# Optimization experiments

Hardware: AMD Instinct MI355X
Metric: run time of the kernel (lower is better)

Reference implementation:

```python
import jax, jax.numpy as jnp
import numpy as np
from jax import lax

DN = ('NCHW', 'OIHW', 'NCHW')


def conv2d(x, w, b, pad):
    y = lax.conv_general_dilated(x, w, (1, 1), [(pad, pad), (pad, pad)], dimension_numbers=DN)
    return y + b[None, :, None, None]


def bilinear_sample(x, py, px):
    # x: [B,C,H,W]; py,px: [B,kk,H,W] fractional sample coords (zero outside).
    B, C, H, W = x.shape
    y0 = jnp.floor(py)
    x0 = jnp.floor(px)
    wy1 = py - y0
    wx1 = px - x0
    wy0 = 1.0 - wy1
    wx0 = 1.0 - wx1
    xf = x.reshape(B, C, H * W)

    def gather(yi, xi):
        valid = (yi >= 0) & (yi <= H - 1) & (xi >= 0) & (xi <= W - 1)
        yc = jnp.clip(yi, 0, H - 1).astype(jnp.int32)
        xc = jnp.clip(xi, 0, W - 1).astype(jnp.int32)
        idx = (yc * W + xc).reshape(B, -1)  # [B, kk*H*W]
        v = jax.vmap(lambda xb, ib: xb[:, ib])(xf, idx)  # [B,C,kk*H*W]
        v = v.reshape(B, C, *yi.shape[1:])
        return v * valid[:, None].astype(x.dtype)

    out = gather(y0, x0) * (wy0 * wx0)[:, None]
    out = out + gather(y0, x0 + 1.0) * (wy0 * wx1)[:, None]
    out = out + gather(y0 + 1.0, x0) * (wy1 * wx0)[:, None]
    out = out + gather(y0 + 1.0, x0 + 1.0) * (wy1 * wx1)[:, None]
    return out  # [B,C,kk,H,W]


def deform_branch(x, w_off, b_off, w_mask, b_mask, w_dcn, k):
    # offset/mask generator convs (kernel k, same padding), then DCNv2-style
    # modulated deformable conv (stride 1, dilation 1, groups 1, no bias).
    pad = k // 2
    kk = k * k
    B, C, H, W = x.shape
    offset = conv2d(x, w_off, b_off, pad)              # [B,2kk,H,W]
    mask = jax.nn.sigmoid(conv2d(x, w_mask, b_mask, pad))  # [B,kk,H,W]
    oy = offset[:, 0::2]  # y offsets per tap  [B,kk,H,W]
    ox = offset[:, 1::2]  # x offsets per tap
    iy, ix = jnp.meshgrid(jnp.arange(k), jnp.arange(k), indexing='ij')
    iy = iy.reshape(-1).astype(x.dtype)  # [kk]
    ix = ix.reshape(-1).astype(x.dtype)
    base_y = jnp.arange(H, dtype=x.dtype)[None, :, None] - pad + iy[:, None, None]  # [kk,H,1]
    base_x = jnp.arange(W, dtype=x.dtype)[None, None, :] - pad + ix[:, None, None]  # [kk,1,W]
    py = base_y[None] + oy  # [B,kk,H,W]
    px = base_x[None] + ox
    samp = bilinear_sample(x, py, px) * mask[:, None]  # [B,C,kk,H,W]
    wf = w_dcn.reshape(w_dcn.shape[0], w_dcn.shape[1], kk)  # [Cout,Cin,kk]
    return jnp.einsum('bckhw,ock->bohw', samp, wf)


def setup_inputs() -> dict:
    key = jax.random.key(0)
    B, Cin, Cout, H, W = 2, 64, 64, 80, 80
    ks = jax.random.split(key, 20)
    inp = {'x': jax.random.normal(ks[0], (B, Cin, H, W), dtype=jnp.float32)}
    i = 1
    for k in (3, 5, 7):
        kk = k * k
        inp[f'w_off{k}'] = jax.random.normal(ks[i], (2 * kk, Cin, k, k), dtype=jnp.float32) * 0.02
        inp[f'b_off{k}'] = jax.random.normal(ks[i + 1], (2 * kk,), dtype=jnp.float32) * 0.1
        inp[f'w_mask{k}'] = jax.random.normal(ks[i + 2], (kk, Cin, k, k), dtype=jnp.float32) * 0.02
        inp[f'b_mask{k}'] = jax.random.normal(ks[i + 3], (kk,), dtype=jnp.float32) * 0.1
        inp[f'w_dcn{k}'] = jax.random.normal(ks[i + 4], (Cout, Cin, k, k), dtype=jnp.float32) * (1.0 / np.sqrt(Cin * kk))
        i += 5
    return inp


def reference(x, w_off3, b_off3, w_mask3, b_mask3, w_dcn3,
              w_off5, b_off5, w_mask5, b_mask5, w_dcn5,
              w_off7, b_off7, w_mask7, b_mask7, w_dcn7):
    p1 = deform_branch(x, w_off3, b_off3, w_mask3, b_mask3, w_dcn3, 3)
    p2 = deform_branch(x, w_off5, b_off5, w_mask5, b_mask5, w_dcn5, 5)
    p3 = deform_branch(x, w_off7, b_off7, w_mask7, b_mask7, w_dcn7, 7)
    return jnp.concatenate([p1, p2, p3], axis=1)
```

## Files before the change

kernel.cpp:

```cpp
#include <hip/hip_runtime.h>
#include <math.h>

constexpr int B = 2, C = 64, H = 80, W = 80, HW = H * W, COUT = 64;
constexpr int NPIX = B * HW;

typedef __attribute__((ext_vector_type(8))) short short8;
typedef __attribute__((ext_vector_type(4))) float f32x4;
typedef __attribute__((ext_vector_type(2))) float f32x2;

__device__ inline ushort f2bf(float f) {
  unsigned u = __float_as_uint(f);
  unsigned r = u + 0x7fff + ((u >> 16) & 1);
  return (ushort)(r >> 16);
}

__device__ inline f32x2 unpack_bf2(unsigned u) {
  f32x2 r;
  r.x = __uint_as_float(u << 16);
  r.y = __uint_as_float(u & 0xffff0000u);
  return r;
}

__device__ inline unsigned bilin_pack(unsigned a, unsigned b, unsigned c,
                                      unsigned d, f32x2 c00, f32x2 c01,
                                      f32x2 c10, f32x2 c11) {
  f32x2 p = unpack_bf2(a) * c00;
  p += unpack_bf2(b) * c01;
  p += unpack_bf2(c) * c10;
  p += unpack_bf2(d) * c11;
  unsigned lo = __float_as_uint(p.x) + 0x8000u;
  unsigned hi = __float_as_uint(p.y) + 0x8000u;
  return __builtin_amdgcn_perm(hi, lo, 0x07060302);
}

__device__ __forceinline__ void gload_lds16(const ushort* g, ushort* s) {
  __builtin_amdgcn_global_load_lds(
      (const __attribute__((address_space(1))) void*)g,
      (__attribute__((address_space(3))) void*)s, 16, 0, 0);
}

template <int K, int NT>
__device__ void prep_body(int pb, int nblk, const float* __restrict__ w_off,
                          const float* __restrict__ b_off,
                          const float* __restrict__ w_mask,
                          const float* __restrict__ b_mask,
                          const float* __restrict__ w_dcn,
                          ushort* __restrict__ wtbs, float* __restrict__ bcomb,
                          ushort* __restrict__ wdts) {
  constexpr int KK = K * K, C3 = 3 * KK;
  const int n1 = KK * 2 * NT * 512;
  const int n2 = C3;
  const int n3 = KK * 2 * 4 * 512;
  const int total = n1 + n2 + n3;
  for (int i = pb * 256 + threadIdx.x; i < total; i += nblk * 256) {
    if (i < n1) {
      int e = i & 7, l = (i >> 3) & 63;
      int blk512 = i >> 9;
      int nt = blk512 % NT, th = blk512 / NT;
      int half = th & 1, t = th >> 1;
      int n = nt * 16 + (l & 15);
      int ci = half * 32 + (l >> 4) * 8 + e;
      float v = 0.f;
      if (n < 2 * KK) v = w_off[(n * C + ci) * KK + t];
      else if (n < C3) v = w_mask[((n - 2 * KK) * C + ci) * KK + t];
      wtbs[i] = f2bf(v);
    } else if (i < n1 + n2) {
      int co = i - n1;
      bcomb[co] = (co < 2 * KK) ? b_off[co] : b_mask[co - 2 * KK];
    } else {
      int j = i - n1 - n2;
      int e = j & 7, l = (j >> 3) & 63;
      int blk512 = j >> 9;
      int jt = blk512 & 3, th = blk512 >> 2;
      int half = th & 1, t = th >> 1;
      int co = jt * 16 + (l & 15);
      int ci = half * 32 + (l >> 4) * 8 + e;
      wdts[j] = f2bf(w_dcn[(co * C + ci) * KK + t]);
    }
  }
}

__global__ __launch_bounds__(256) void setup_all(
    const float* __restrict__ x, ushort* __restrict__ xhb,
    const float* __restrict__ w_off3, const float* __restrict__ b_off3,
    const float* __restrict__ w_mask3, const float* __restrict__ b_mask3,
    const float* __restrict__ w_dcn3, ushort* __restrict__ wtbs3,
    float* __restrict__ bc3, ushort* __restrict__ wdts3,
    const float* __restrict__ w_off5, const float* __restrict__ b_off5,
    const float* __restrict__ w_mask5, const float* __restrict__ b_mask5,
    const float* __restrict__ w_dcn5, ushort* __restrict__ wtbs5,
    float* __restrict__ bc5, ushort* __restrict__ wdts5,
    const float* __restrict__ w_off7, const float* __restrict__ b_off7,
    const float* __restrict__ w_mask7, const float* __restrict__ b_mask7,
    const float* __restrict__ w_dcn7, ushort* __restrict__ wtbs7,
    float* __restrict__ bc7, ushort* __restrict__ wdts7) {
  __shared__ float tile[64][65];
  int blk = blockIdx.x;
  if (blk < 200) {
    int b = blk / (HW / 64);
    int p0 = (blk % (HW / 64)) * 64;
    int lane = threadIdx.x & 63, row = threadIdx.x >> 6;
    if (blk == 0) {
      for (int i = threadIdx.x; i < 640; i += 256)
        xhb[(size_t)B * HW * C + i] = 0;
    }
#pragma unroll
    for (int it = 0; it < 16; ++it) {
      int ci = it * 4 + row;
      tile[ci][lane] = x[(size_t)(b * C + ci) * HW + p0 + lane];
    }
    __syncthreads();
#pragma unroll
    for (int it = 0; it < 16; ++it) {
      int pl = it * 4 + row;
      xhb[((size_t)b * HW + p0 + pl) * C + lane] = f2bf(tile[lane][pl]);
    }
  } else {
    int pb = blk - 200;
    prep_body<7, 10>(pb, 256, w_off7, b_off7, w_mask7, b_mask7, w_dcn7, wtbs7,
                     bc7, wdts7);
    prep_body<5, 6>(pb, 256, w_off5, b_off5, w_mask5, b_mask5, w_dcn5, wtbs5,
                    bc5, wdts5);
    prep_body<3, 2>(pb, 256, w_off3, b_off3, w_mask3, b_mask3, w_dcn3, wtbs3,
                    bc3, wdts3);
  }
}

template <int K, int NT>
__device__ __forceinline__ void conv_body(int blk,
                                          const ushort* __restrict__ xhb,
                                          const ushort* __restrict__ zsrc,
                                          const ushort* __restrict__ wtbs,
                                          const float* __restrict__ bcomb,
                                          float* __restrict__ convout,
                                          ushort* win) {
  constexpr int PAD = K / 2, KK = K * K, C3 = 3 * KK;
  int tid = threadIdx.x, w = tid >> 6, l = tid & 63;
  int lm = l & 15, lk = l >> 4;
  int m0 = blk * 16;
  int b = m0 / HW;
  int rem = m0 % HW;
  int y = rem / W, x0 = rem % W;
  int xs = x0 - 4;

  for (int i = w; i < K * 3; i += 4) {
    int r = i / 3, sgm = i % 3;
    int gy = y - PAD + r;
    int px = xs + sgm * 8 + (l >> 3);
    bool v = ((unsigned)gy < (unsigned)H) && ((unsigned)px < (unsigned)W);
    int slot = (l & 7) ^ ((4 + (l >> 3)) & 7);
    const ushort* src =
        v ? (xhb + ((size_t)b * HW + gy * W + px) * C + slot * 8)
          : (zsrc + l * 8);
    gload_lds16(src, win + (r * 24 + sgm * 8) * 64);
  }
  asm volatile("s_waitcnt vmcnt(0)" ::: "memory");
  __syncthreads();

  int j0w, ntw;
  if constexpr (K == 7) { j0w = (w < 2) ? w * 3 : 6 + (w - 2) * 2; ntw = (w < 2) ? 3 : 2; }
  else if constexpr (K == 5) { j0w = (w < 2) ? w * 2 : 4 + (w - 2); ntw = (w < 2) ? 2 : 1; }
  else { j0w = (w < 2) ? w : 0; ntw = (w < 2) ? 1 : 0; }

  f32x4 acc[3];
#pragma unroll
  for (int j = 0; j < 3; ++j) acc[j] = f32x4{0.f, 0.f, 0.f, 0.f};

  short8 Bf0[2][3], Bf1[2][3];
  auto loadB = [&](int t, int s) {
    const ushort* fbase = wtbs + (size_t)(t * 2) * NT * 512 + l * 8;
#pragma unroll
    for (int jj = 0; jj < 3; ++jj)
      if (jj < ntw) {
        Bf0[s][jj] = *(const short8*)(fbase + (size_t)(j0w + jj) * 512);
        Bf1[s][jj] = *(const short8*)(fbase + (size_t)(NT + j0w + jj) * 512);
      }
  };

  loadB(0, 0);
#pragma unroll
  for (int t = 0; t < KK; ++t) {
    int s = t & 1;
    if (t + 1 < KK) loadB(t + 1, s ^ 1);
    int ky = t / K, kx = t % K;
    int c = 4 + lm + kx - PAD;
    int h = (4 + c) & 7;
    const ushort* ap = win + (ky * 24 + c) * 64;
    short8 A0v = *(const short8*)(ap + ((lk ^ h) * 8));
    short8 A1v = *(const short8*)(ap + (((lk + 4) ^ h) * 8));
#pragma unroll
    for (int jj = 0; jj < 3; ++jj)
      if (jj < ntw)
        acc[jj] = __builtin_amdgcn_mfma_f32_16x16x32_bf16(A0v, Bf0[s][jj],
                                                          acc[jj], 0, 0, 0);
#pragma unroll
    for (int jj = 0; jj < 3; ++jj)
      if (jj < ntw)
        acc[jj] = __builtin_amdgcn_mfma_f32_16x16x32_bf16(A1v, Bf1[s][jj],
                                                          acc[jj], 0, 0, 0);
  }

#pragma unroll
  for (int jj = 0; jj < 3; ++jj) {
    if (jj >= ntw) continue;
    int co = (j0w + jj) * 16 + lm;
    if (co >= C3) continue;
    float bs = bcomb[co];
    bool isoff = co < 2 * KK;
    int tp = isoff ? (co >> 1) : (co - 2 * KK);
    int plane = isoff ? (co & 1) : 2;
    f32x4 vv;
#pragma unroll
    for (int r = 0; r < 4; ++r) {
      int xr = x0 + lk * 4 + r;
      float v = acc[jj][r] + bs;
      if (isoff) {
        v += (co & 1) ? (float)(xr - PAD + tp % K)
                      : (float)(y - PAD + tp / K);
      } else {
        v = 1.f / (1.f + expf(-v));
      }
      vv[r] = v;
    }
    int pix0 = m0 + lk * 4;
    *(f32x4*)(convout + ((size_t)plane * KK + tp) * NPIX + pix0) = vv;
  }
}

__global__ __launch_bounds__(256, 4) void conv_all(
    const ushort* __restrict__ xhb,
    const ushort* __restrict__ wtbs7, const float* __restrict__ bc7, float* __restrict__ co7,
    const ushort* __restrict__ wtbs5, const float* __restrict__ bc5, float* __restrict__ co5,
    const ushort* __restrict__ wtbs3, const float* __restrict__ bc3, float* __restrict__ co3) {
  __shared__ ushort win[7 * 24 * 64];
  const ushort* zsrc = xhb + (size_t)B * HW * C;
  int blk = blockIdx.x;
  if (blk < 800) conv_body<7, 10>(blk, xhb, zsrc, wtbs7, bc7, co7, win);
  else if (blk < 1600) conv_body<5, 6>(blk - 800, xhb, zsrc, wtbs5, bc5, co5, win);
  else conv_body<3, 2>(blk - 1600, xhb, zsrc, wtbs3, bc3, co3, win);
}

template <int K, int TPW>
__device__ __forceinline__ void dcn_body(int blk, const ushort* __restrict__ xhb,
                                         const float* __restrict__ convout,
                                         const ushort* __restrict__ wdts,
                                         float* __restrict__ out, int br_off,
                                         float* smem) {
  constexpr int KK = K * K;
  int tid = threadIdx.x, w = tid >> 6, l = tid & 63;
  int lm = l & 15, lk = l >> 4;
  int m0 = blk * 32;
  int b = m0 / HW;
  const ushort* xb = xhb + (size_t)b * HW * C;
  const float* pyP = convout;
  const float* pxP = convout + (size_t)KK * NPIX;
  const float* mP = convout + (size_t)2 * KK * NPIX;
  const int t0 = w * TPW;

  f32x4 acc[2][4];
#pragma unroll
  for (int g = 0; g < 2; ++g)
#pragma unroll
    for (int j = 0; j < 4; ++j) acc[g][j] = f32x4{0.f, 0.f, 0.f, 0.f};

  float pvy = 0.f, pvx = 0.f, pvm = 0.f;
  auto lofs = [&](int tt) {
    int t = t0 + tt;
    bool tv = t < KK;
    int ts = tv ? t : KK - 1;
    if (l < 32) {
      size_t o = (size_t)ts * NPIX + m0 + l;
      pvy = pyP[o];
      pvx = pxP[o];
      pvm = tv ? mP[o] : 0.f;
    }
  };

  auto sample = [&](float py, float px, float m, uint4 (&U)[8],
                    f32x2 (&CCv)[4]) {
    float fy = floorf(py), fx = floorf(px);
    float wy1 = py - fy, wx1 = px - fx;
    float wy0 = 1.f - wy1, wx0 = 1.f - wx1;
    int y0 = (int)fy, x0 = (int)fx;
    int y1 = y0 + 1, x1 = x0 + 1;
    bool vy0 = (unsigned)y0 < (unsigned)H, vy1 = (unsigned)y1 < (unsigned)H;
    bool vx0 = (unsigned)x0 < (unsigned)W, vx1 = (unsigned)x1 < (unsigned)W;
    float c00s = m * wy0 * wx0 * ((vy0 & vx0) ? 1.f : 0.f);
    float c01s = m * wy0 * wx1 * ((vy0 & vx1) ? 1.f : 0.f);
    float c10s = m * wy1 * wx0 * ((vy1 & vx0) ? 1.f : 0.f);
    float c11s = m * wy1 * wx1 * ((vy1 & vx1) ? 1.f : 0.f);
    CCv[0] = f32x2{c00s, c00s};
    CCv[1] = f32x2{c01s, c01s};
    CCv[2] = f32x2{c10s, c10s};
    CCv[3] = f32x2{c11s, c11s};
    int y0c = min(max(y0, 0), H - 1), y1c = min(max(y1, 0), H - 1);
    int x0c = min(max(x0, 0), W - 1), x1c = min(max(x1, 0), W - 1);
    int i00 = (y0c * W + x0c) * C + lk * 8, i01 = (y0c * W + x1c) * C + lk * 8;
    int i10 = (y1c * W + x0c) * C + lk * 8, i11 = (y1c * W + x1c) * C + lk * 8;
    U[0] = *(const uint4*)(xb + i00);
    U[1] = *(const uint4*)(xb + i00 + 32);
    U[2] = *(const uint4*)(xb + i01);
    U[3] = *(const uint4*)(xb + i01 + 32);
    U[4] = *(const uint4*)(xb + i10);
    U[5] = *(const uint4*)(xb + i10 + 32);
    U[6] = *(const uint4*)(xb + i11);
    U[7] = *(const uint4*)(xb + i11 + 32);
  };

  auto pack2 = [&](uint4 (&U)[8], f32x2 (&CCv)[4], short8& aa, short8& ab) {
    f32x2 c00 = CCv[0], c01 = CCv[1], c10 = CCv[2], c11 = CCv[3];
    uint4 apa, apb;
    apa.x = bilin_pack(U[0].x, U[2].x, U[4].x, U[6].x, c00, c01, c10, c11);
    apa.y = bilin_pack(U[0].y, U[2].y, U[4].y, U[6].y, c00, c01, c10, c11);
    apa.z = bilin_pack(U[0].z, U[2].z, U[4].z, U[6].z, c00, c01, c10, c11);
    apa.w = bilin_pack(U[0].w, U[2].w, U[4].w, U[6].w, c00, c01, c10, c11);
    apb.x = bilin_pack(U[1].x, U[3].x, U[5].x, U[7].x, c00, c01, c10, c11);
    apb.y = bilin_pack(U[1].y, U[3].y, U[5].y, U[7].y, c00, c01, c10, c11);
    apb.z = bilin_pack(U[1].z, U[3].z, U[5].z, U[7].z, c00, c01, c10, c11);
    apb.w = bilin_pack(U[1].w, U[3].w, U[5].w, U[7].w, c00, c01, c10, c11);
    aa = *(short8*)&apa;
    ab = *(short8*)&apb;
  };

  lofs(0);
#pragma unroll
  for (int tt = 0; tt < TPW; ++tt) {
    float pyA = __shfl(pvy, lm), pyB = __shfl(pvy, lm + 16);
    float pxA = __shfl(pvx, lm), pxB = __shfl(pvx, lm + 16);
    float mA = __shfl(pvm, lm), mB = __shfl(pvm, lm + 16);
    int ts = min(t0 + tt, KK - 1);
    if (tt + 1 < TPW) lofs(tt + 1);

    uint4 UA[8], UB[8];
    f32x2 CA[4], CB[4];
    sample(pyA, pxA, mA, UA, CA);
    sample(pyB, pxB, mB, UB, CB);
    short8 aaA, abA, aaB, abB;
    pack2(UA, CA, aaA, abA);
    pack2(UB, CB, aaB, abB);

    const ushort* fb0 = wdts + (size_t)((ts * 2 + 0) * 4) * 512 + l * 8;
    const ushort* fb1 = wdts + (size_t)((ts * 2 + 1) * 4) * 512 + l * 8;
#pragma unroll
    for (int j = 0; j < 4; ++j) {
      short8 bf = *(const short8*)(fb0 + j * 512);
      acc[0][j] = __builtin_amdgcn_mfma_f32_16x16x32_bf16(aaA, bf, acc[0][j], 0, 0, 0);
      acc[1][j] = __builtin_amdgcn_mfma_f32_16x16x32_bf16(aaB, bf, acc[1][j], 0, 0, 0);
    }
#pragma unroll
    for (int j = 0; j < 4; ++j) {
      short8 bf = *(const short8*)(fb1 + j * 512);
      acc[0][j] = __builtin_amdgcn_mfma_f32_16x16x32_bf16(abA, bf, acc[0][j], 0, 0, 0);
      acc[1][j] = __builtin_amdgcn_mfma_f32_16x16x32_bf16(abB, bf, acc[1][j], 0, 0, 0);
    }
  }

  float (*s_red)[32][65] = (float (*)[32][65])smem;
#pragma unroll
  for (int g = 0; g < 2; ++g)
#pragma unroll
    for (int j = 0; j < 4; ++j)
#pragma unroll
      for (int r = 0; r < 4; ++r)
        s_red[w][g * 16 + lk * 4 + r][j * 16 + lm] = acc[g][j][r];
  __syncthreads();
  int rem0 = m0 - b * HW;
#pragma unroll
  for (int i = 0; i < 8; ++i) {
    int idx = i * 256 + tid;
    int mrow = idx & 31, co = idx >> 5;
    float v = s_red[0][mrow][co] + s_red[1][mrow][co] +
              s_red[2][mrow][co] + s_red[3][mrow][co];
    out[(size_t)(b * (3 * COUT) + br_off + co) * HW + rem0 + mrow] = v;
  }
}

__global__ __launch_bounds__(256, 3) void dcn_all(
    const ushort* __restrict__ xhb,
    const float* __restrict__ co7, const ushort* __restrict__ wdts7,
    const float* __restrict__ co5, const ushort* __restrict__ wdts5,
    const float* __restrict__ co3, const ushort* __restrict__ wdts3,
    float* __restrict__ out) {
  __shared__ float smem[4 * 32 * 65];
  int blk = blockIdx.x;
  if (blk < 400) dcn_body<7, 13>(blk, xhb, co7, wdts7, out, 128, smem);
  else if (blk < 800) dcn_body<5, 7>(blk - 400, xhb, co5, wdts5, out, 64, smem);
  else dcn_body<3, 3>(blk - 800, xhb, co3, wdts3, out, 0, smem);
}

extern "C" void kernel_launch(void* const* d_in, const int* in_sizes, int n_in,
                              void* d_out, int out_size, void* d_ws,
                              size_t ws_size, hipStream_t stream) {
  const float* x = (const float*)d_in[0];
  const float* w_off3 = (const float*)d_in[1];
  const float* b_off3 = (const float*)d_in[2];
  const float* w_mask3 = (const float*)d_in[3];
  const float* b_mask3 = (const float*)d_in[4];
  const float* w_dcn3 = (const float*)d_in[5];
  const float* w_off5 = (const float*)d_in[6];
  const float* b_off5 = (const float*)d_in[7];
  const float* w_mask5 = (const float*)d_in[8];
  const float* b_mask5 = (const float*)d_in[9];
  const float* w_dcn5 = (const float*)d_in[10];
  const float* w_off7 = (const float*)d_in[11];
  const float* b_off7 = (const float*)d_in[12];
  const float* w_mask7 = (const float*)d_in[13];
  const float* b_mask7 = (const float*)d_in[14];
  const float* w_dcn7 = (const float*)d_in[15];
  float* out = (float*)d_out;
  float* ws = (float*)d_ws;

  size_t off = 0;
  auto alloc = [&](size_t n) {
    size_t p = off;
    off += (n + 3) & ~(size_t)3;
    return ws + p;
  };
  ushort* xhb = (ushort*)alloc((size_t)B * HW * C / 2 + 320);
  float* co3 = alloc((size_t)B * HW * 27);
  float* co5 = alloc((size_t)B * HW * 75);
  float* co7 = alloc((size_t)B * HW * 147);
  ushort* wtbs3 = (ushort*)alloc(9 * 2 * 2 * 512 / 2);
  ushort* wtbs5 = (ushort*)alloc(25 * 2 * 6 * 512 / 2);
  ushort* wtbs7 = (ushort*)alloc(49 * 2 * 10 * 512 / 2);
  float* bc3 = alloc(27);
  float* bc5 = alloc(75);
  float* bc7 = alloc(147);
  ushort* wdts3 = (ushort*)alloc(9 * 2 * 4 * 512 / 2);
  ushort* wdts5 = (ushort*)alloc(25 * 2 * 4 * 512 / 2);
  ushort* wdts7 = (ushort*)alloc(49 * 2 * 4 * 512 / 2);

  setup_all<<<456, 256, 0, stream>>>(
      x, xhb,
      w_off3, b_off3, w_mask3, b_mask3, w_dcn3, wtbs3, bc3, wdts3,
      w_off5, b_off5, w_mask5, b_mask5, w_dcn5, wtbs5, bc5, wdts5,
      w_off7, b_off7, w_mask7, b_mask7, w_dcn7, wtbs7, bc7, wdts7);

  conv_all<<<2400, 256, 0, stream>>>(xhb, wtbs7, bc7, co7, wtbs5, bc5, co5,
                                     wtbs3, bc3, co3);

  dcn_all<<<1200, 256, 0, stream>>>(xhb, co7, wdts7, co5, wdts5, co3, wdts3,
                                    out);
}
```

Before: 220.4 us.

## Process both batch images per conv block to reuse weight fragments

Each offset/mask conv block now handles the same 16-pixel tile for both batch images. It loads two input windows into LDS and reuses each loaded weight fragment for two MFMA groups, which halves the grid and the global weight traffic. The 5x5 branch weight padding drops from 6 to 5 N-tiles, which removes a wasted tile. In exchange the block uses double the LDS and more accumulator registers, so occupancy is lowered to 3 blocks per CU.

```diff
diff --git a/kernel.cpp b/kernel.cpp
--- a/kernel.cpp
+++ b/kernel.cpp
@@ -119,58 +119,66 @@
     int pb = blk - 200;
     prep_body<7, 10>(pb, 256, w_off7, b_off7, w_mask7, b_mask7, w_dcn7, wtbs7,
                      bc7, wdts7);
-    prep_body<5, 6>(pb, 256, w_off5, b_off5, w_mask5, b_mask5, w_dcn5, wtbs5,
+    prep_body<5, 5>(pb, 256, w_off5, b_off5, w_mask5, b_mask5, w_dcn5, wtbs5,
                     bc5, wdts5);
     prep_body<3, 2>(pb, 256, w_off3, b_off3, w_mask3, b_mask3, w_dcn3, wtbs3,
                     bc3, wdts3);
   }
 }
 
-template <int K, int NT>
-__device__ __forceinline__ void conv_body(int blk,
-                                          const ushort* __restrict__ xhb,
-                                          const ushort* __restrict__ zsrc,
-                                          const ushort* __restrict__ wtbs,
-                                          const float* __restrict__ bcomb,
-                                          float* __restrict__ convout,
-                                          ushort* win) {
+template <int K, int NT, int NMAX>
+__device__ __forceinline__ void conv_body32(int blk,
+                                            const ushort* __restrict__ xhb,
+                                            const ushort* __restrict__ zsrc,
+                                            const ushort* __restrict__ wtbs,
+                                            const float* __restrict__ bcomb,
+                                            float* __restrict__ convout,
+                                            ushort* win) {
   constexpr int PAD = K / 2, KK = K * K, C3 = 3 * KK;
+  constexpr int WSZ = K * 24 * 64;
   int tid = threadIdx.x, w = tid >> 6, l = tid & 63;
   int lm = l & 15, lk = l >> 4;
-  int m0 = blk * 16;
-  int b = m0 / HW;
-  int rem = m0 % HW;
-  int y = rem / W, x0 = rem % W;
+  int y = blk / 5, x0 = (blk % 5) * 16;
   int xs = x0 - 4;
 
-  for (int i = w; i < K * 3; i += 4) {
-    int r = i / 3, sgm = i % 3;
+  for (int i = w; i < 2 * K * 3; i += 4) {
+    int wb = i / (K * 3), j = i % (K * 3);
+    int r = j / 3, sgm = j % 3;
     int gy = y - PAD + r;
     int px = xs + sgm * 8 + (l >> 3);
     bool v = ((unsigned)gy < (unsigned)H) && ((unsigned)px < (unsigned)W);
     int slot = (l & 7) ^ ((4 + (l >> 3)) & 7);
     const ushort* src =
-        v ? (xhb + ((size_t)b * HW + gy * W + px) * C + slot * 8)
+        v ? (xhb + ((size_t)wb * HW + gy * W + px) * C + slot * 8)
           : (zsrc + l * 8);
-    gload_lds16(src, win + (r * 24 + sgm * 8) * 64);
+    gload_lds16(src, win + wb * WSZ + (r * 24 + sgm * 8) * 64);
   }
   asm volatile("s_waitcnt vmcnt(0)" ::: "memory");
   __syncthreads();
 
   int j0w, ntw;
-  if constexpr (K == 7) { j0w = (w < 2) ? w * 3 : 6 + (w - 2) * 2; ntw = (w < 2) ? 3 : 2; }
-  else if constexpr (K == 5) { j0w = (w < 2) ? w * 2 : 4 + (w - 2); ntw = (w < 2) ? 2 : 1; }
-  else { j0w = (w < 2) ? w : 0; ntw = (w < 2) ? 1 : 0; }
-
-  f32x4 acc[3];
-#pragma unroll
-  for (int j = 0; j < 3; ++j) acc[j] = f32x4{0.f, 0.f, 0.f, 0.f};
-
-  short8 Bf0[2][3], Bf1[2][3];
+  if constexpr (K == 7) {
+    const int J0[4] = {0, 3, 6, 8}, NW[4] = {3, 3, 2, 2};
+    j0w = J0[w]; ntw = NW[w];
+  } else if constexpr (K == 5) {
+    const int J0[4] = {0, 2, 3, 4}, NW[4] = {2, 1, 1, 1};
+    j0w = J0[w]; ntw = NW[w];
+  } else {
+    const int J0[4] = {0, 1, 0, 0}, NW[4] = {1, 1, 0, 0};
+    j0w = J0[w]; ntw = NW[w];
+  }
+
+  f32x4 acc[2][NMAX];
+#pragma unroll
+  for (int g = 0; g < 2; ++g)
+#pragma unroll
+    for (int j = 0; j < NMAX; ++j) acc[g][j] = f32x4{0.f, 0.f, 0.f, 0.f};
+
+  short8 Bf0[2][NMAX], Bf1[2][NMAX];
   auto loadB = [&](int t, int s) {
     const ushort* fbase = wtbs + (size_t)(t * 2) * NT * 512 + l * 8;
 #pragma unroll
-    for (int jj = 0; jj < 3; ++jj)
+    for (int jj = 0; jj < NMAX; ++jj)
       if (jj < ntw) {
         Bf0[s][jj] = *(const short8*)(fbase + (size_t)(j0w + jj) * 512);
         Bf1[s][jj] = *(const short8*)(fbase + (size_t)(NT + j0w + jj) * 512);
@@ -185,59 +193,65 @@
     int ky = t / K, kx = t % K;
     int c = 4 + lm + kx - PAD;
     int h = (4 + c) & 7;
-    const ushort* ap = win + (ky * 24 + c) * 64;
-    short8 A0v = *(const short8*)(ap + ((lk ^ h) * 8));
-    short8 A1v = *(const short8*)(ap + (((lk + 4) ^ h) * 8));
-#pragma unroll
-    for (int jj = 0; jj < 3; ++jj)
-      if (jj < ntw)
-        acc[jj] = __builtin_amdgcn_mfma_f32_16x16x32_bf16(A0v, Bf0[s][jj],
-                                                          acc[jj], 0, 0, 0);
-#pragma unroll
-    for (int jj = 0; jj < 3; ++jj)
-      if (jj < ntw)
-        acc[jj] = __builtin_amdgcn_mfma_f32_16x16x32_bf16(A1v, Bf1[s][jj],
-                                                          acc[jj], 0, 0, 0);
-  }
-
-#pragma unroll
-  for (int jj = 0; jj < 3; ++jj) {
-    if (jj >= ntw) continue;
-    int co = (j0w + jj) * 16 + lm;
-    if (co >= C3) continue;
-    float bs = bcomb[co];
-    bool isoff = co < 2 * KK;
-    int tp = isoff ? (co >> 1) : (co - 2 * KK);
-    int plane = isoff ? (co & 1) : 2;
-    f32x4 vv;
-#pragma unroll
-    for (int r = 0; r < 4; ++r) {
-      int xr = x0 + lk * 4 + r;
-      float v = acc[jj][r] + bs;
-      if (isoff) {
-        v += (co & 1) ? (float)(xr - PAD + tp % K)
-                      : (float)(y - PAD + tp / K);
-      } else {
-        v = 1.f / (1.f + expf(-v));
+#pragma unroll
+    for (int g = 0; g < 2; ++g) {
+      const ushort* ap = win + g * WSZ + (ky * 24 + c) * 64;
+      short8 A0v = *(const short8*)(ap + ((lk ^ h) * 8));
+      short8 A1v = *(const short8*)(ap + (((lk + 4) ^ h) * 8));
+#pragma unroll
+      for (int jj = 0; jj < NMAX; ++jj)
+        if (jj < ntw)
+          acc[g][jj] = __builtin_amdgcn_mfma_f32_16x16x32_bf16(
+              A0v, Bf0[s][jj], acc[g][jj], 0, 0, 0);
+#pragma unroll
+      for (int jj = 0; jj < NMAX; ++jj)
+        if (jj < ntw)
+          acc[g][jj] = __builtin_amdgcn_mfma_f32_16x16x32_bf16(
+              A1v, Bf1[s][jj], acc[g][jj], 0, 0, 0);
+    }
+  }
+
+#pragma unroll
+  for (int g = 0; g < 2; ++g) {
+#pragma unroll
+    for (int jj = 0; jj < NMAX; ++jj) {
+      if (jj >= ntw) continue;
+      int co = (j0w + jj) * 16 + lm;
+      if (co >= C3) continue;
+      float bs = bcomb[co];
+      bool isoff = co < 2 * KK;
+      int tp = isoff ? (co >> 1) : (co - 2 * KK);
+      int plane = isoff ? (co & 1) : 2;
+      f32x4 vv;
+#pragma unroll
+      for (int r = 0; r < 4; ++r) {
+        int xr = x0 + lk * 4 + r;
+        float v = acc[g][jj][r] + bs;
+        if (isoff) {
+          v += (co & 1) ? (float)(xr - PAD + tp % K)
+                        : (float)(y - PAD + tp / K);
+        } else {
+          v = 1.f / (1.f + expf(-v));
+        }
+        vv[r] = v;
       }
-      vv[r] = v;
-    }
-    int pix0 = m0 + lk * 4;
-    *(f32x4*)(convout + ((size_t)plane * KK + tp) * NPIX + pix0) = vv;
-  }
-}
-
-__global__ __launch_bounds__(256, 4) void conv_all(
+      int pix0 = g * HW + blk * 16 + lk * 4;
+      *(f32x4*)(convout + ((size_t)plane * KK + tp) * NPIX + pix0) = vv;
+    }
+  }
+}
+
+__global__ __launch_bounds__(256, 3) void conv_all(
     const ushort* __restrict__ xhb,
     const ushort* __restrict__ wtbs7, const float* __restrict__ bc7, float* __restrict__ co7,
     const ushort* __restrict__ wtbs5, const float* __restrict__ bc5, float* __restrict__ co5,
     const ushort* __restrict__ wtbs3, const float* __restrict__ bc3, float* __restrict__ co3) {
-  __shared__ ushort win[7 * 24 * 64];
+  __shared__ ushort win[2 * 7 * 24 * 64];
   const ushort* zsrc = xhb + (size_t)B * HW * C;
   int blk = blockIdx.x;
-  if (blk < 800) conv_body<7, 10>(blk, xhb, zsrc, wtbs7, bc7, co7, win);
-  else if (blk < 1600) conv_body<5, 6>(blk - 800, xhb, zsrc, wtbs5, bc5, co5, win);
-  else conv_body<3, 2>(blk - 1600, xhb, zsrc, wtbs3, bc3, co3, win);
+  if (blk < 400) conv_body32<7, 10, 3>(blk, xhb, zsrc, wtbs7, bc7, co7, win);
+  else if (blk < 800) conv_body32<5, 5, 2>(blk - 400, xhb, zsrc, wtbs5, bc5, co5, win);
+  else conv_body32<3, 2, 1>(blk - 800, xhb, zsrc, wtbs3, bc3, co3, win);
 }
 
 template <int K, int TPW>
@@ -421,7 +435,7 @@
   float* co5 = alloc((size_t)B * HW * 75);
   float* co7 = alloc((size_t)B * HW * 147);
   ushort* wtbs3 = (ushort*)alloc(9 * 2 * 2 * 512 / 2);
-  ushort* wtbs5 = (ushort*)alloc(25 * 2 * 6 * 512 / 2);
+  ushort* wtbs5 = (ushort*)alloc(25 * 2 * 5 * 512 / 2);
   ushort* wtbs7 = (ushort*)alloc(49 * 2 * 10 * 512 / 2);
   float* bc3 = alloc(27);
   float* bc5 = alloc(75);
@@ -436,7 +450,7 @@
       w_off5, b_off5, w_mask5, b_mask5, w_dcn5, wtbs5, bc5, wdts5,
       w_off7, b_off7, w_mask7, b_mask7, w_dcn7, wtbs7, bc7, wdts7);
 
-  conv_all<<<2400, 256, 0, stream>>>(xhb, wtbs7, bc7, co7, wtbs5, bc5, co5,
+  conv_all<<<1200, 256, 0, stream>>>(xhb, wtbs7, bc7, co7, wtbs5, bc5, co5,
                                      wtbs3, bc3, co3);
 
   dcn_all<<<1200, 256, 0, stream>>>(xhb, co7, wdts7, co5, wdts5, co3, wdts3,
```

Result: faster. 203.2 us (-7.8%).
